# Optimization experiments

Hardware: AMD Instinct MI355X
Metric: run time of the kernel (lower is better)

The kernel has to match this reference:

```python
import math
import jax, jax.numpy as jnp
import numpy as np

B, L, D, H = 2, 2048, 1024, 16
HD = D // H
EPS = 1e-6
ROPE_BASE = 10000.0


def setup_inputs() -> dict:
    key = jax.random.key(0)
    ks = jax.random.split(key, 6)
    s = 0.02
    return {
        "z_H_previous": jax.random.normal(ks[0], (B, L, D), jnp.float32),
        "z_L_current": jax.random.normal(ks[1], (B, L, D), jnp.float32),
        "w_qkv": jax.random.normal(ks[2], (3 * D, D), jnp.float32) * s,
        "w_out": jax.random.normal(ks[3], (D, D), jnp.float32) * s,
        "w_ffn1": jax.random.normal(ks[4], (4 * D, D), jnp.float32) * s,
        "w_ffn2": jax.random.normal(ks[5], (D, 4 * D), jnp.float32) * s,
        "g_norm1": jnp.ones((D,), jnp.float32),
        "g_norm2": jnp.ones((D,), jnp.float32),
    }


def _rmsnorm(x, g):
    # mean of squares over last dim, rsqrt, scale
    ms = jnp.mean(x * x, axis=-1, keepdims=True)
    return x * jax.lax.rsqrt(ms + EPS) * g


def _rope(x):
    # x: [b, h, l, hd]; non-interleaved rotate-half RoPE
    l, d = x.shape[-2], x.shape[-1]
    half = d // 2
    inv_freq = 1.0 / (ROPE_BASE ** (jnp.arange(half, dtype=jnp.float32) / half))
    freqs = jnp.arange(l, dtype=jnp.float32)[:, None] * inv_freq[None, :]  # [l, half]
    cos, sin = jnp.cos(freqs), jnp.sin(freqs)
    x1, x2 = x[..., :half], x[..., half:]
    return jnp.concatenate([x1 * cos - x2 * sin, x2 * cos + x1 * sin], axis=-1)


def reference(z_H_previous, z_L_current, w_qkv, w_out, w_ffn1, w_ffn2, g_norm1, g_norm2):
    x = z_H_previous + z_L_current                       # [b, l, d]
    h = _rmsnorm(x, g_norm1)
    b, l, d = h.shape
    qkv = h @ w_qkv.T                                    # [b, l, 3d]
    qkv = qkv.reshape(b, l, 3, H, HD).transpose(2, 0, 3, 1, 4)  # [3, b, h, l, hd]
    q, k, v = qkv[0], qkv[1], qkv[2]
    q = _rope(q)
    k = _rope(k)
    scores = jnp.einsum("bhqd,bhkd->bhqk", q, k) / math.sqrt(HD)
    attn = jax.nn.softmax(scores, axis=-1)
    out = jnp.einsum("bhqk,bhkd->bhqd", attn, v)         # [b, h, l, hd]
    out = out.transpose(0, 2, 1, 3).reshape(b, l, d)
    x = x + out @ w_out.T
    h2 = _rmsnorm(x, g_norm2)
    ffn = jax.nn.silu(h2 @ w_ffn1.T) @ w_ffn2.T
    return x + ffn
```

## Files before the change

### kernel.cpp

```cpp
#include <hip/hip_runtime.h>

typedef __bf16 bf16;
typedef __bf16 bf16x2 __attribute__((ext_vector_type(2)));
typedef __bf16 bf16x8 __attribute__((ext_vector_type(8)));
typedef __bf16 bf16x4 __attribute__((ext_vector_type(4)));
typedef float  f32x4  __attribute__((ext_vector_type(4)));
typedef float  f32x16 __attribute__((ext_vector_type(16)));
typedef unsigned int uint;

static __device__ __forceinline__ void async_copy16(const void* g, void* l) {
  __builtin_amdgcn_global_load_lds((__attribute__((address_space(1))) void*)g,
                                   (__attribute__((address_space(3))) void*)l,
                                   16, 0, 0);
}

static __device__ __forceinline__ uint pkbf2(float a, float b) {
  union { bf16x2 v; uint u; } x;
  x.v[0] = (bf16)a; x.v[1] = (bf16)b;
  return x.u;
}

union U4 { uint u[4]; bf16x8 v; };

__global__ __launch_bounds__(256) void f2b_kernel(const float* __restrict__ in,
                                                  bf16* __restrict__ out, int n4) {
  int i = blockIdx.x * 256 + threadIdx.x;
  if (i < n4) {
    float4 v = ((const float4*)in)[i];
    bf16x4 o;
    o[0] = (bf16)v.x; o[1] = (bf16)v.y; o[2] = (bf16)v.z; o[3] = (bf16)v.w;
    ((bf16x4*)out)[i] = o;
  }
}

__global__ __launch_bounds__(256)
void add_rmsnorm_kernel(const float* __restrict__ a, const float* __restrict__ b,
                        const float* __restrict__ g, float* __restrict__ xout,
                        bf16* __restrict__ hout) {
  const int row = blockIdx.x;
  const int tid = threadIdx.x;
  const size_t base = (size_t)row * 1024 + tid * 4;
  float4 x = *(const float4*)(a + base);
  if (b) {
    float4 y = *(const float4*)(b + base);
    x.x += y.x; x.y += y.y; x.z += y.z; x.w += y.w;
  }
  float ss = x.x*x.x + x.y*x.y + x.z*x.z + x.w*x.w;
#pragma unroll
  for (int off = 32; off > 0; off >>= 1) ss += __shfl_xor(ss, off, 64);
  __shared__ float red[4];
  const int wave = tid >> 6, lane = tid & 63;
  if (lane == 0) red[wave] = ss;
  __syncthreads();
  const float total = red[0] + red[1] + red[2] + red[3];
  const float scale = rsqrtf(total * (1.0f / 1024.0f) + 1e-6f);
  if (xout) *(float4*)(xout + base) = x;
  float4 gv = *(const float4*)(g + tid * 4);
  bf16x4 h;
  h[0] = (bf16)(x.x * scale * gv.x);
  h[1] = (bf16)(x.y * scale * gv.y);
  h[2] = (bf16)(x.z * scale * gv.z);
  h[3] = (bf16)(x.w * scale * gv.w);
  *(bf16x4*)(hout + base) = h;
}

__global__ __launch_bounds__(256) void rope_kernel(bf16* __restrict__ qk) {
  int idx = blockIdx.x * 256 + threadIdx.x;
  const int hd = idx & 31; idx >>= 5;
  const int l  = idx & 2047; idx >>= 11;
  const int h  = idx & 15; idx >>= 4;
  const int b  = idx & 1;  idx >>= 1;
  bf16* p = qk + (size_t)idx * 4194304 + ((size_t)(b * 16 + h) * 2048 + l) * 64;
  const float inv = powf(10000.0f, -(float)hd * (1.0f / 32.0f));
  const float fr = (float)l * inv;
  float s, c; sincosf(fr, &s, &c);
  const float x1 = (float)p[hd], x2 = (float)p[hd + 32];
  p[hd]      = (bf16)(x1 * c - x2 * s);
  p[hd + 32] = (bf16)(x2 * c + x1 * s);
}

enum { EP_QKV = 0, EP_ADD_RESID = 1, EP_SILU = 2 };

template <int MODE>
__global__ __launch_bounds__(256)
void gemm_bt(const bf16* __restrict__ A, const bf16* __restrict__ W,
             const float* __restrict__ resid, float* __restrict__ outF,
             bf16* __restrict__ outB, bf16* __restrict__ outB2,
             int M, int N, int K) {
  __shared__ bf16 As[128 * 64];
  __shared__ bf16 Bs[128 * 64];
  const int tid  = threadIdx.x;
  const int wave = tid >> 6;
  const int lane = tid & 63;
  const int quad = lane >> 4;
  const int l16  = lane & 15;

  const int bm = blockIdx.x & 31;
  const int bn = blockIdx.x >> 5;
  const int m0 = bm << 7, n0 = bn << 7;
  const int wm = (wave >> 1) << 6;
  const int wn = (wave & 1) << 6;

  const int rl = lane >> 3;
  const int cg = (lane & 7) ^ rl;
  const bf16* gA = A + (size_t)(m0 + wave * 32 + rl) * K + cg * 8;
  const bf16* gB = W + (size_t)(n0 + wave * 32 + rl) * K + cg * 8;

  const int s8 = l16 & 7;
  f32x4 acc[4][4] = {};

  for (int k0 = 0; k0 < K; k0 += 64) {
    __syncthreads();
#pragma unroll
    for (int i = 0; i < 4; i++) {
      async_copy16(gA + (size_t)(i * 8) * K, &As[(wave * 32 + i * 8) * 64]);
      async_copy16(gB + (size_t)(i * 8) * K, &Bs[(wave * 32 + i * 8) * 64]);
    }
    gA += 64; gB += 64;
    __syncthreads();
#pragma unroll
    for (int kh = 0; kh < 2; kh++) {
      bf16x8 af[4], bfr[4];
#pragma unroll
      for (int i = 0; i < 4; i++)
        af[i] = *(const bf16x8*)&As[(wm + i * 16 + l16) * 64 + (((kh * 4 + quad) ^ s8) * 8)];
#pragma unroll
      for (int j = 0; j < 4; j++)
        bfr[j] = *(const bf16x8*)&Bs[(wn + j * 16 + l16) * 64 + (((kh * 4 + quad) ^ s8) * 8)];
#pragma unroll
      for (int i = 0; i < 4; i++)
#pragma unroll
        for (int j = 0; j < 4; j++)
          acc[i][j] = __builtin_amdgcn_mfma_f32_16x16x32_bf16(af[i], bfr[j], acc[i][j], 0, 0, 0);
    }
  }

#pragma unroll
  for (int i = 0; i < 4; i++) {
    const int mbase = m0 + wm + i * 16 + quad * 4;
#pragma unroll
    for (int j = 0; j < 4; j++) {
      const int n = n0 + wn + j * 16 + l16;
      f32x4 v = acc[i][j];
#pragma unroll
      for (int r = 0; r < 4; r++) {
        const int m = mbase + r;
        const float val = v[r];
        if constexpr (MODE == EP_QKV) {
          const int bb = m >> 11, l = m & 2047;
          const int which = n >> 10, hh = (n >> 6) & 15, hd = n & 63;
          if (which == 2) {
            outB2[((size_t)(bb * 16 + hh) * 64 + hd) * 2048 + l] = (bf16)val;
          } else {
            const float sc = (which == 0) ? 0.1803368801111243f : 1.0f;
            outB[(((size_t)(which * 2 + bb) * 16 + hh) * 2048 + l) * 64 + hd] = (bf16)(val * sc);
          }
        } else if constexpr (MODE == EP_ADD_RESID) {
          outF[(size_t)m * N + n] = val + resid[(size_t)m * N + n];
        } else {
          outB[(size_t)m * N + n] = (bf16)(val / (1.0f + __expf(-val)));
        }
      }
    }
  }
}

__global__ __launch_bounds__(256)
void gemm_bt_splitk(const bf16* __restrict__ A, const bf16* __restrict__ W,
                    float* __restrict__ P, int M, int N, int Ktot) {
  __shared__ bf16 As[128 * 64];
  __shared__ bf16 Bs[128 * 64];
  const int tid  = threadIdx.x;
  const int wave = tid >> 6;
  const int lane = tid & 63;
  const int quad = lane >> 4;
  const int l16  = lane & 15;

  const int r6 = blockIdx.x & 63;
  const int bn = blockIdx.x >> 6;
  const int bm = r6 >> 1;
  const int split = r6 & 1;
  const int m0 = bm << 7, n0 = bn << 7;
  const int wm = (wave >> 1) << 6;
  const int wn = (wave & 1) << 6;
  const int Kh = Ktot >> 1;
  const int koff = split * Kh;

  const int rl = lane >> 3;
  const int cg = (lane & 7) ^ rl;
  const bf16* gA = A + (size_t)(m0 + wave * 32 + rl) * Ktot + koff + cg * 8;
  const bf16* gB = W + (size_t)(n0 + wave * 32 + rl) * Ktot + koff + cg * 8;

  const int s8 = l16 & 7;
  f32x4 acc[4][4] = {};

  for (int k0 = 0; k0 < Kh; k0 += 64) {
    __syncthreads();
#pragma unroll
    for (int i = 0; i < 4; i++) {
      async_copy16(gA + (size_t)(i * 8) * Ktot, &As[(wave * 32 + i * 8) * 64]);
      async_copy16(gB + (size_t)(i * 8) * Ktot, &Bs[(wave * 32 + i * 8) * 64]);
    }
    gA += 64; gB += 64;
    __syncthreads();
#pragma unroll
    for (int kh = 0; kh < 2; kh++) {
      bf16x8 af[4], bfr[4];
#pragma unroll
      for (int i = 0; i < 4; i++)
        af[i] = *(const bf16x8*)&As[(wm + i * 16 + l16) * 64 + (((kh * 4 + quad) ^ s8) * 8)];
#pragma unroll
      for (int j = 0; j < 4; j++)
        bfr[j] = *(const bf16x8*)&Bs[(wn + j * 16 + l16) * 64 + (((kh * 4 + quad) ^ s8) * 8)];
#pragma unroll
      for (int i = 0; i < 4; i++)
#pragma unroll
        for (int j = 0; j < 4; j++)
          acc[i][j] = __builtin_amdgcn_mfma_f32_16x16x32_bf16(af[i], bfr[j], acc[i][j], 0, 0, 0);
    }
  }

  float* Pd = P + (size_t)split * M * N;
#pragma unroll
  for (int i = 0; i < 4; i++) {
    const int mbase = m0 + wm + i * 16 + quad * 4;
#pragma unroll
    for (int j = 0; j < 4; j++) {
      const int n = n0 + wn + j * 16 + l16;
#pragma unroll
      for (int r = 0; r < 4; r++)
        Pd[(size_t)(mbase + r) * N + n] = acc[i][j][r];
    }
  }
}

__global__ __launch_bounds__(256)
void splitk_combine(const float* __restrict__ P, const float* __restrict__ resid,
                    float* __restrict__ out, int total4) {
  int i = blockIdx.x * 256 + threadIdx.x;
  if (i < total4) {
    float4 a = ((const float4*)P)[i];
    float4 b = ((const float4*)(P + 4194304))[i];
    float4 r = ((const float4*)resid)[i];
    float4 o;
    o.x = a.x + b.x + r.x; o.y = a.y + b.y + r.y;
    o.z = a.z + b.z + r.z; o.w = a.w + b.w + r.w;
    ((float4*)out)[i] = o;
  }
}

__global__ __launch_bounds__(256)
void gemm64_bt(const bf16* __restrict__ A, const bf16* __restrict__ W,
               const float* __restrict__ resid, float* __restrict__ outF,
               int M, int N, int K) {
  __shared__ bf16 As[64 * 64];
  __shared__ bf16 Bs[128 * 64];
  const int tid = threadIdx.x, wave = tid >> 6, lane = tid & 63;
  const int quad = lane >> 4, l16 = lane & 15;
  const int bm = blockIdx.x & 63;
  const int bn = blockIdx.x >> 6;
  const int m0 = bm << 6, n0 = bn << 7;
  const int wm = (wave >> 1) * 32, wn = (wave & 1) * 64;

  const int rl = lane >> 3;
  const int cg = (lane & 7) ^ rl;
  const bf16* gA = A + (size_t)(m0 + wave * 16 + rl) * K + cg * 8;
  const bf16* gB = W + (size_t)(n0 + wave * 32 + rl) * K + cg * 8;

  const int s8 = l16 & 7;
  f32x4 acc[2][4] = {};
  for (int k0 = 0; k0 < K; k0 += 64) {
    __syncthreads();
#pragma unroll
    for (int i = 0; i < 2; i++)
      async_copy16(gA + (size_t)(i * 8) * K, &As[(wave * 16 + i * 8) * 64]);
#pragma unroll
    for (int i = 0; i < 4; i++)
      async_copy16(gB + (size_t)(i * 8) * K, &Bs[(wave * 32 + i * 8) * 64]);
    gA += 64; gB += 64;
    __syncthreads();
#pragma unroll
    for (int kh = 0; kh < 2; kh++) {
      bf16x8 af[2], bfr[4];
#pragma unroll
      for (int i = 0; i < 2; i++)
        af[i] = *(const bf16x8*)&As[(wm + i * 16 + l16) * 64 + (((kh * 4 + quad) ^ s8) * 8)];
#pragma unroll
      for (int j = 0; j < 4; j++)
        bfr[j] = *(const bf16x8*)&Bs[(wn + j * 16 + l16) * 64 + (((kh * 4 + quad) ^ s8) * 8)];
#pragma unroll
      for (int i = 0; i < 2; i++)
#pragma unroll
        for (int j = 0; j < 4; j++)
          acc[i][j] = __builtin_amdgcn_mfma_f32_16x16x32_bf16(af[i], bfr[j], acc[i][j], 0, 0, 0);
    }
  }
#pragma unroll
  for (int i = 0; i < 2; i++) {
    const int mbase = m0 + wm + i * 16 + quad * 4;
#pragma unroll
    for (int j = 0; j < 4; j++) {
      const int n = n0 + wn + j * 16 + l16;
#pragma unroll
      for (int r = 0; r < 4; r++) {
        const int m = mbase + r;
        outF[(size_t)m * N + n] = acc[i][j][r] + resid[(size_t)m * N + n];
      }
    }
  }
}

__global__ __launch_bounds__(256, 4)
void attn_kernel(const bf16* __restrict__ qk, const bf16* __restrict__ vt,
                 bf16* __restrict__ Opart, float* __restrict__ Lpart) {
  const int qt    = blockIdx.x & 15;
  const int bh    = (blockIdx.x >> 4) & 31;
  const int split = blockIdx.x >> 9;
  const bf16* Qp = qk + (size_t)bh * 131072;
  const bf16* Kp = Qp + 4194304;
  const bf16* Vp = vt + (size_t)bh * 131072;

  const int tid = threadIdx.x, wave = tid >> 6, lane = tid & 63;
  const int hl = lane >> 5, l32 = lane & 31;
  const int qw = qt * 128 + wave * 32;

  __shared__ bf16 lds[9216];
  bf16* Ks = lds;
  bf16* Vs = lds + 4096;

  bf16x8 qf[4];
#pragma unroll
  for (int dk = 0; dk < 4; dk++)
    qf[dk] = *(const bf16x8*)&Qp[(size_t)(qw + l32) * 64 + dk * 16 + hl * 8];

  f32x16 o0 = {}, o1 = {};
  float l_i = 0.0f;

  const int rl = lane >> 3;
  const int cg = (lane & 7) ^ rl;

  const int kvbase = split * 512;
  for (int kv0 = kvbase; kv0 < kvbase + 512; kv0 += 64) {
    __syncthreads();
#pragma unroll
    for (int i = 0; i < 2; i++) {
      const int row = wave * 16 + i * 8;
      async_copy16(Kp + (size_t)(kv0 + row + rl) * 64 + cg * 8, &Ks[row * 64]);
      async_copy16(Vp + (size_t)(row + rl) * 2048 + kv0 + cg * 8, &Vs[row * 64]);
    }
    __syncthreads();

    f32x16 s0 = {}, s1 = {};
#pragma unroll
    for (int dk = 0; dk < 4; dk++) {
      const bf16x8 kf = *(const bf16x8*)&Ks[l32 * 64 + ((dk * 2 + hl) ^ (l32 & 7)) * 8];
      s0 = __builtin_amdgcn_mfma_f32_32x32x16_bf16(kf, qf[dk], s0, 0, 0, 0);
    }
#pragma unroll
    for (int dk = 0; dk < 4; dk++) {
      const bf16x8 kf = *(const bf16x8*)&Ks[(32 + l32) * 64 + ((dk * 2 + hl) ^ (l32 & 7)) * 8];
      s1 = __builtin_amdgcn_mfma_f32_32x32x16_bf16(kf, qf[dk], s1, 0, 0, 0);
    }

    U4 pf[4];
    float sum = 0.0f;
#pragma unroll
    for (int ks = 0; ks < 2; ks++) {
      const f32x16 sv = ks ? s1 : s0;
      uint d[8];
#pragma unroll
      for (int i = 0; i < 8; i++) {
        const float a = exp2f(sv[2 * i]);
        const float b = exp2f(sv[2 * i + 1]);
        sum += a + b;
        d[i] = pkbf2(a, b);
      }
      uint send0 = hl ? d[0] : d[2];
      uint send1 = hl ? d[1] : d[3];
      uint send2 = hl ? d[4] : d[6];
      uint send3 = hl ? d[5] : d[7];
      const uint r0 = __shfl_xor(send0, 32, 64);
      const uint r1 = __shfl_xor(send1, 32, 64);
      const uint r2 = __shfl_xor(send2, 32, 64);
      const uint r3 = __shfl_xor(send3, 32, 64);
      U4& f0 = pf[ks * 2];
      U4& f1 = pf[ks * 2 + 1];
      f0.u[0] = hl ? r0 : d[0];  f0.u[1] = hl ? r1 : d[1];
      f0.u[2] = hl ? d[2] : r0;  f0.u[3] = hl ? d[3] : r1;
      f1.u[0] = hl ? r2 : d[4];  f1.u[1] = hl ? r3 : d[5];
      f1.u[2] = hl ? d[6] : r2;  f1.u[3] = hl ? d[7] : r3;
    }
    l_i += sum + __shfl_xor(sum, 32, 64);

#pragma unroll
    for (int c16 = 0; c16 < 4; c16++) {
      const bf16x8 vf0 = *(const bf16x8*)&Vs[l32 * 64 + ((c16 * 2 + hl) ^ (l32 & 7)) * 8];
      const bf16x8 vf1 = *(const bf16x8*)&Vs[(32 + l32) * 64 + ((c16 * 2 + hl) ^ (l32 & 7)) * 8];
      o0 = __builtin_amdgcn_mfma_f32_32x32x16_bf16(vf0, pf[c16].v, o0, 0, 0, 0);
      o1 = __builtin_amdgcn_mfma_f32_32x32x16_bf16(vf1, pf[c16].v, o1, 0, 0, 0);
    }
  }

  Lpart[(size_t)(split * 32 + bh) * 2048 + qt * 128 + wave * 32 + l32] = l_i;

  __syncthreads();
  uint* L32 = (uint*)lds;
  const int qloc = wave * 32 + l32;
#pragma unroll
  for (int ds = 0; ds < 2; ds++) {
    const f32x16 ov = ds ? o1 : o0;
#pragma unroll
    for (int i = 0; i < 8; i++) {
      const int r = 2 * i;
      const int dd = ds * 32 + (r & 3) + 8 * (r >> 2) + 4 * hl;
      L32[qloc * 36 + (dd >> 1)] = pkbf2(ov[r], ov[r + 1]);
    }
  }
  __syncthreads();
#pragma unroll
  for (int p = 0; p < 4; p++) {
    const int qr = p * 32 + (tid >> 3), c = tid & 7;
    const uint4 v = *(const uint4*)&L32[qr * 36 + c * 4];
    *(uint4*)&Opart[(((size_t)(split * 32 + bh) * 2048) + qt * 128 + qr) * 64 + c * 8] = v;
  }
}

__global__ __launch_bounds__(256)
void attn_combine(const bf16* __restrict__ Opart, const float* __restrict__ Lpart,
                  bf16* __restrict__ out) {
  const int t = blockIdx.x * 256 + threadIdx.x;
  const int c = t & 7, qq = t >> 3;
  const int bh = qq >> 11, q = qq & 2047;
  const int b = bh >> 4, h = bh & 15;
  float acc[8] = {};
  float lsum = 0.0f;
#pragma unroll
  for (int s = 0; s < 4; s++) {
    const bf16x8 ov = *(const bf16x8*)&Opart[((size_t)(s * 32 + bh) * 2048 + q) * 64 + c * 8];
    lsum += Lpart[(size_t)(s * 32 + bh) * 2048 + q];
#pragma unroll
    for (int i = 0; i < 8; i++) acc[i] += (float)ov[i];
  }
  const float inv = 1.0f / lsum;
  bf16x8 o;
#pragma unroll
  for (int i = 0; i < 8; i++) o[i] = (bf16)(acc[i] * inv);
  *(bf16x8*)&out[((size_t)b * 2048 + q) * 1024 + h * 64 + c * 8] = o;
}

extern "C" void kernel_launch(void* const* d_in, const int* in_sizes, int n_in,
                              void* d_out, int out_size, void* d_ws, size_t ws_size,
                              hipStream_t stream) {
  (void)in_sizes; (void)n_in; (void)out_size; (void)ws_size;
  const float* zH    = (const float*)d_in[0];
  const float* zL    = (const float*)d_in[1];
  const float* w_qkv = (const float*)d_in[2];
  const float* w_out = (const float*)d_in[3];
  const float* w_f1  = (const float*)d_in[4];
  const float* w_f2  = (const float*)d_in[5];
  const float* g1    = (const float*)d_in[6];
  const float* g2    = (const float*)d_in[7];
  float* out = (float*)d_out;

  char* ws = (char*)d_ws;
  size_t off = 0;
  auto alloc = [&](size_t bytes) {
    void* p = ws + off;
    off += (bytes + 255) & ~(size_t)255;
    return p;
  };
  bf16*  bqkv  = (bf16*)alloc(3145728ull * 2);
  bf16*  bwout = (bf16*)alloc(1048576ull * 2);
  bf16*  bf1   = (bf16*)alloc(4194304ull * 2);
  bf16*  bf2   = (bf16*)alloc(4194304ull * 2);
  const size_t off_x = off;
  float* x     = (float*)alloc(4194304ull * 4);
  bf16*  hbuf  = (bf16*)alloc(4194304ull * 2);
  bf16*  qkb   = (bf16*)alloc(8388608ull * 2);
  bf16*  vtb   = (bf16*)alloc(4194304ull * 2);
  bf16*  attnb = (bf16*)alloc(4194304ull * 2);
  const size_t offU = off;
  float* x2    = (float*)alloc(4194304ull * 4);
  bf16*  h2    = (bf16*)alloc(4194304ull * 2);
  bf16*  act   = (bf16*)alloc(16777216ull * 2);
  bf16*  Opart = (bf16*)(ws + offU);
  float* Lpart = (float*)(ws + offU + 16777216ull * 2 + 256);
  float* Ppart = (float*)(ws + off_x);

  f2b_kernel<<<3072, 256, 0, stream>>>(w_qkv, bqkv, 3145728 / 4);
  f2b_kernel<<<1024, 256, 0, stream>>>(w_out, bwout, 1048576 / 4);
  f2b_kernel<<<4096, 256, 0, stream>>>(w_f1, bf1, 4194304 / 4);
  f2b_kernel<<<4096, 256, 0, stream>>>(w_f2, bf2, 4194304 / 4);

  add_rmsnorm_kernel<<<4096, 256, 0, stream>>>(zH, zL, g1, x, hbuf);

  gemm_bt<EP_QKV><<<768, 256, 0, stream>>>(hbuf, bqkv, nullptr, nullptr, qkb, vtb,
                                           4096, 3072, 1024);
  rope_kernel<<<16384, 256, 0, stream>>>(qkb);
  attn_kernel<<<2048, 256, 0, stream>>>(qkb, vtb, Opart, Lpart);
  attn_combine<<<2048, 256, 0, stream>>>(Opart, Lpart, attnb);

  gemm64_bt<<<512, 256, 0, stream>>>(attnb, bwout, x, x2, 4096, 1024, 1024);
  add_rmsnorm_kernel<<<4096, 256, 0, stream>>>(x2, nullptr, g2, nullptr, h2);
  gemm_bt<EP_SILU><<<1024, 256, 0, stream>>>(h2, bf1, nullptr, nullptr, act, nullptr,
                                             4096, 4096, 1024);
  gemm_bt_splitk<<<512, 256, 0, stream>>>(act, bf2, Ppart, 4096, 1024, 4096);
  splitk_combine<<<4096, 256, 0, stream>>>(Ppart, x2, out, 1048576);
}
```

Before: 380.0 us.

## Fuse RoPE into QKV epilogue, merge weight casts, trim attention LDS

Applies rotary embedding directly in the QKV GEMM epilogue by pairing accumulator columns hd and hd+32, which removes the separate rope kernel and its read-modify-write pass over Q and K. The four weight-conversion launches become one combined kernel. The attention kernel computes scores one half at a time to reduce live registers, moves the row-sum shuffle out of the loop, and writes its output through LDS in two passes so the shared buffer shrinks to 8192 elements. Rotation is now applied before bf16 rounding, which changes numerics slightly, and sincos runs per element in the epilogue.

After: 372.0 us. -2.1%, faster.

```diff
diff --git a/kernel.cpp b/kernel.cpp
--- a/kernel.cpp
+++ b/kernel.cpp
@@ -22,15 +22,21 @@
 
 union U4 { uint u[4]; bf16x8 v; };
 
-__global__ __launch_bounds__(256) void f2b_kernel(const float* __restrict__ in,
-                                                  bf16* __restrict__ out, int n4) {
+__global__ __launch_bounds__(256)
+void f2b_all(const float* __restrict__ s0, const float* __restrict__ s1,
+             const float* __restrict__ s2, const float* __restrict__ s3,
+             bf16* __restrict__ d0, bf16* __restrict__ d1,
+             bf16* __restrict__ d2, bf16* __restrict__ d3) {
   int i = blockIdx.x * 256 + threadIdx.x;
-  if (i < n4) {
-    float4 v = ((const float4*)in)[i];
-    bf16x4 o;
-    o[0] = (bf16)v.x; o[1] = (bf16)v.y; o[2] = (bf16)v.z; o[3] = (bf16)v.w;
-    ((bf16x4*)out)[i] = o;
-  }
+  const float* s; bf16* d; int j;
+  if (i < 786432)       { s = s0; d = d0; j = i; }
+  else if (i < 1048576) { s = s1; d = d1; j = i - 786432; }
+  else if (i < 2097152) { s = s2; d = d2; j = i - 1048576; }
+  else                  { s = s3; d = d3; j = i - 2097152; }
+  float4 v = ((const float4*)s)[j];
+  bf16x4 o;
+  o[0] = (bf16)v.x; o[1] = (bf16)v.y; o[2] = (bf16)v.z; o[3] = (bf16)v.w;
+  ((bf16x4*)d)[j] = o;
 }
 
 __global__ __launch_bounds__(256)
@@ -64,21 +70,6 @@
   *(bf16x4*)(hout + base) = h;
 }
 
-__global__ __launch_bounds__(256) void rope_kernel(bf16* __restrict__ qk) {
-  int idx = blockIdx.x * 256 + threadIdx.x;
-  const int hd = idx & 31; idx >>= 5;
-  const int l  = idx & 2047; idx >>= 11;
-  const int h  = idx & 15; idx >>= 4;
-  const int b  = idx & 1;  idx >>= 1;
-  bf16* p = qk + (size_t)idx * 4194304 + ((size_t)(b * 16 + h) * 2048 + l) * 64;
-  const float inv = powf(10000.0f, -(float)hd * (1.0f / 32.0f));
-  const float fr = (float)l * inv;
-  float s, c; sincosf(fr, &s, &c);
-  const float x1 = (float)p[hd], x2 = (float)p[hd + 32];
-  p[hd]      = (bf16)(x1 * c - x2 * s);
-  p[hd + 32] = (bf16)(x2 * c + x1 * s);
-}
-
 enum { EP_QKV = 0, EP_ADD_RESID = 1, EP_SILU = 2 };
 
 template <int MODE>
@@ -135,30 +126,66 @@
     }
   }
 
-#pragma unroll
-  for (int i = 0; i < 4; i++) {
-    const int mbase = m0 + wm + i * 16 + quad * 4;
-#pragma unroll
-    for (int j = 0; j < 4; j++) {
-      const int n = n0 + wn + j * 16 + l16;
-      f32x4 v = acc[i][j];
-#pragma unroll
-      for (int r = 0; r < 4; r++) {
-        const int m = mbase + r;
-        const float val = v[r];
-        if constexpr (MODE == EP_QKV) {
-          const int bb = m >> 11, l = m & 2047;
-          const int which = n >> 10, hh = (n >> 6) & 15, hd = n & 63;
-          if (which == 2) {
-            outB2[((size_t)(bb * 16 + hh) * 64 + hd) * 2048 + l] = (bf16)val;
+  if constexpr (MODE == EP_QKV) {
+    const int which = n0 >> 10;
+    if (which == 2) {
+#pragma unroll
+      for (int i = 0; i < 4; i++) {
+        const int mbase = m0 + wm + i * 16 + quad * 4;
+#pragma unroll
+        for (int j = 0; j < 4; j++) {
+          const int n = n0 + wn + j * 16 + l16;
+          const int hh = (n >> 6) & 15, hd = n & 63;
+#pragma unroll
+          for (int r = 0; r < 4; r++) {
+            const int m = mbase + r;
+            const int bb = m >> 11, l = m & 2047;
+            outB2[((size_t)(bb * 16 + hh) * 64 + hd) * 2048 + l] = (bf16)acc[i][j][r];
+          }
+        }
+      }
+    } else {
+      const float sc = (which == 0) ? 0.1803368801111243f : 1.0f;
+#pragma unroll
+      for (int jp = 0; jp < 2; jp++) {
+        const int hd1 = jp * 16 + l16;
+        const float invf = exp2f(-0.4152410118609203f * (float)hd1);
+        const int n1 = n0 + wn + jp * 16 + l16;
+        const int hh = (n1 >> 6) & 15;
+#pragma unroll
+        for (int i = 0; i < 4; i++) {
+          const int mbase = m0 + wm + i * 16 + quad * 4;
+#pragma unroll
+          for (int r = 0; r < 4; r++) {
+            const int m = mbase + r;
+            const int bb = m >> 11, l = m & 2047;
+            float sv, cv;
+            sincosf((float)l * invf, &sv, &cv);
+            const float x1 = acc[i][jp][r], x2 = acc[i][jp + 2][r];
+            const size_t base = (((size_t)(which * 2 + bb) * 16 + hh) * 2048 + l) * 64;
+            outB[base + hd1]      = (bf16)((x1 * cv - x2 * sv) * sc);
+            outB[base + hd1 + 32] = (bf16)((x2 * cv + x1 * sv) * sc);
+          }
+        }
+      }
+    }
+  } else {
+#pragma unroll
+    for (int i = 0; i < 4; i++) {
+      const int mbase = m0 + wm + i * 16 + quad * 4;
+#pragma unroll
+      for (int j = 0; j < 4; j++) {
+        const int n = n0 + wn + j * 16 + l16;
+        f32x4 v = acc[i][j];
+#pragma unroll
+        for (int r = 0; r < 4; r++) {
+          const int m = mbase + r;
+          const float val = v[r];
+          if constexpr (MODE == EP_ADD_RESID) {
+            outF[(size_t)m * N + n] = val + resid[(size_t)m * N + n];
           } else {
-            const float sc = (which == 0) ? 0.1803368801111243f : 1.0f;
-            outB[(((size_t)(which * 2 + bb) * 16 + hh) * 2048 + l) * 64 + hd] = (bf16)(val * sc);
+            outB[(size_t)m * N + n] = (bf16)(val / (1.0f + __expf(-val)));
           }
-        } else if constexpr (MODE == EP_ADD_RESID) {
-          outF[(size_t)m * N + n] = val + resid[(size_t)m * N + n];
-        } else {
-          outB[(size_t)m * N + n] = (bf16)(val / (1.0f + __expf(-val)));
         }
       }
     }
@@ -324,7 +351,7 @@
   const int hl = lane >> 5, l32 = lane & 31;
   const int qw = qt * 128 + wave * 32;
 
-  __shared__ bf16 lds[9216];
+  __shared__ bf16 lds[8192];
   bf16* Ks = lds;
   bf16* Vs = lds + 4096;
 
@@ -334,7 +361,7 @@
     qf[dk] = *(const bf16x8*)&Qp[(size_t)(qw + l32) * 64 + dk * 16 + hl * 8];
 
   f32x16 o0 = {}, o1 = {};
-  float l_i = 0.0f;
+  float sum_acc = 0.0f;
 
   const int rl = lane >> 3;
   const int cg = (lane & 7) ^ rl;
@@ -350,29 +377,22 @@
     }
     __syncthreads();
 
-    f32x16 s0 = {}, s1 = {};
-#pragma unroll
-    for (int dk = 0; dk < 4; dk++) {
-      const bf16x8 kf = *(const bf16x8*)&Ks[l32 * 64 + ((dk * 2 + hl) ^ (l32 & 7)) * 8];
-      s0 = __builtin_amdgcn_mfma_f32_32x32x16_bf16(kf, qf[dk], s0, 0, 0, 0);
-    }
-#pragma unroll
-    for (int dk = 0; dk < 4; dk++) {
-      const bf16x8 kf = *(const bf16x8*)&Ks[(32 + l32) * 64 + ((dk * 2 + hl) ^ (l32 & 7)) * 8];
-      s1 = __builtin_amdgcn_mfma_f32_32x32x16_bf16(kf, qf[dk], s1, 0, 0, 0);
-    }
-
     U4 pf[4];
-    float sum = 0.0f;
 #pragma unroll
     for (int ks = 0; ks < 2; ks++) {
-      const f32x16 sv = ks ? s1 : s0;
+      f32x16 s = {};
+#pragma unroll
+      for (int dk = 0; dk < 4; dk++) {
+        const bf16x8 kf = *(const bf16x8*)
+            &Ks[(ks * 32 + l32) * 64 + ((dk * 2 + hl) ^ (l32 & 7)) * 8];
+        s = __builtin_amdgcn_mfma_f32_32x32x16_bf16(kf, qf[dk], s, 0, 0, 0);
+      }
       uint d[8];
 #pragma unroll
       for (int i = 0; i < 8; i++) {
-        const float a = exp2f(sv[2 * i]);
-        const float b = exp2f(sv[2 * i + 1]);
-        sum += a + b;
+        const float a = exp2f(s[2 * i]);
+        const float b = exp2f(s[2 * i + 1]);
+        sum_acc += a + b;
         d[i] = pkbf2(a, b);
       }
       uint send0 = hl ? d[0] : d[2];
@@ -390,7 +410,6 @@
       f1.u[0] = hl ? r2 : d[4];  f1.u[1] = hl ? r3 : d[5];
       f1.u[2] = hl ? d[6] : r2;  f1.u[3] = hl ? d[7] : r3;
     }
-    l_i += sum + __shfl_xor(sum, 32, 64);
 
 #pragma unroll
     for (int c16 = 0; c16 < 4; c16++) {
@@ -401,27 +420,33 @@
     }
   }
 
+  const float l_i = sum_acc + __shfl_xor(sum_acc, 32, 64);
   Lpart[(size_t)(split * 32 + bh) * 2048 + qt * 128 + wave * 32 + l32] = l_i;
 
-  __syncthreads();
   uint* L32 = (uint*)lds;
-  const int qloc = wave * 32 + l32;
-#pragma unroll
-  for (int ds = 0; ds < 2; ds++) {
-    const f32x16 ov = ds ? o1 : o0;
-#pragma unroll
-    for (int i = 0; i < 8; i++) {
-      const int r = 2 * i;
-      const int dd = ds * 32 + (r & 3) + 8 * (r >> 2) + 4 * hl;
-      L32[qloc * 36 + (dd >> 1)] = pkbf2(ov[r], ov[r + 1]);
-    }
-  }
-  __syncthreads();
-#pragma unroll
-  for (int p = 0; p < 4; p++) {
-    const int qr = p * 32 + (tid >> 3), c = tid & 7;
-    const uint4 v = *(const uint4*)&L32[qr * 36 + c * 4];
-    *(uint4*)&Opart[(((size_t)(split * 32 + bh) * 2048) + qt * 128 + qr) * 64 + c * 8] = v;
+#pragma unroll
+  for (int p = 0; p < 2; p++) {
+    __syncthreads();
+    if ((wave >> 1) == p) {
+      const int lrow = (wave & 1) * 32 + l32;
+#pragma unroll
+      for (int ds = 0; ds < 2; ds++) {
+        const f32x16 ov = ds ? o1 : o0;
+#pragma unroll
+        for (int i = 0; i < 8; i++) {
+          const int r = 2 * i;
+          const int dd = ds * 32 + (r & 3) + 8 * (r >> 2) + 4 * hl;
+          L32[lrow * 36 + (dd >> 1)] = pkbf2(ov[r], ov[r + 1]);
+        }
+      }
+    }
+    __syncthreads();
+#pragma unroll
+    for (int sp = 0; sp < 2; sp++) {
+      const int qr = sp * 32 + (tid >> 3), c = tid & 7;
+      const uint4 v = *(const uint4*)&L32[qr * 36 + c * 4];
+      *(uint4*)&Opart[(((size_t)(split * 32 + bh) * 2048) + qt * 128 + p * 64 + qr) * 64 + c * 8] = v;
+    }
   }
 }
 
@@ -487,16 +512,12 @@
   float* Lpart = (float*)(ws + offU + 16777216ull * 2 + 256);
   float* Ppart = (float*)(ws + off_x);
 
-  f2b_kernel<<<3072, 256, 0, stream>>>(w_qkv, bqkv, 3145728 / 4);
-  f2b_kernel<<<1024, 256, 0, stream>>>(w_out, bwout, 1048576 / 4);
-  f2b_kernel<<<4096, 256, 0, stream>>>(w_f1, bf1, 4194304 / 4);
-  f2b_kernel<<<4096, 256, 0, stream>>>(w_f2, bf2, 4194304 / 4);
+  f2b_all<<<12288, 256, 0, stream>>>(w_qkv, w_out, w_f1, w_f2, bqkv, bwout, bf1, bf2);
 
   add_rmsnorm_kernel<<<4096, 256, 0, stream>>>(zH, zL, g1, x, hbuf);
 
   gemm_bt<EP_QKV><<<768, 256, 0, stream>>>(hbuf, bqkv, nullptr, nullptr, qkb, vtb,
                                            4096, 3072, 1024);
-  rope_kernel<<<16384, 256, 0, stream>>>(qkb);
   attn_kernel<<<2048, 256, 0, stream>>>(qkb, vtb, Opart, Lpart);
   attn_combine<<<2048, 256, 0, stream>>>(Opart, Lpart, attnb);
 
```
